# Kernel tuning notes

Measured on AMD Instinct MI355X. Metric: run time of the kernel, lower is better.

Reference implementation:

```python
import jax, jax.numpy as jnp
import numpy as np

DIM = 1024
NUM_HEADS = 16
HEAD_DIM = DIM // NUM_HEADS
SCALE = HEAD_DIM ** -0.5


def setup_inputs() -> dict:
    key = jax.random.key(0)
    ks = jax.random.split(key, 5)
    B, N, C = 2, 2048, DIM
    x = jax.random.normal(ks[0], (B, N, C), dtype=jnp.float32)
    s = 1.0 / np.sqrt(C)
    W_qkv = jax.random.normal(ks[1], (C, 3 * C), dtype=jnp.float32) * s
    b_qkv = jax.random.normal(ks[2], (3 * C,), dtype=jnp.float32) * 0.01
    W_proj = jax.random.normal(ks[3], (C, C), dtype=jnp.float32) * s
    b_proj = jax.random.normal(ks[4], (C,), dtype=jnp.float32) * 0.01
    return {"x": x, "W_qkv": W_qkv, "b_qkv": b_qkv, "W_proj": W_proj, "b_proj": b_proj}


def reference(x, W_qkv, b_qkv, W_proj, b_proj):
    B, N, C = x.shape
    qkv = x @ W_qkv + b_qkv                      # [B, N, 3C]
    qkv = qkv.reshape(B, N, 3, NUM_HEADS, HEAD_DIM)
    qkv = jnp.transpose(qkv, (2, 0, 3, 1, 4))    # [3, B, H, N, hd]
    # Faithful to source quirk: q = k = v = qkv[2]
    v = qkv[2]
    q = v
    k = v
    attn = jnp.einsum('bhnd,bhmd->bhnm', q, k) * SCALE
    attn = jax.nn.softmax(attn, axis=-1)
    out = jnp.einsum('bhnm,bhmd->bhnd', attn, v)  # [B, H, N, hd]
    out = jnp.transpose(out, (0, 2, 1, 3)).reshape(B, N, C)
    return out @ W_proj + b_proj
```

## Files before the change

kernel.cpp:

```cpp
#include <hip/hip_runtime.h>

typedef __bf16    bf16x4 __attribute__((ext_vector_type(4)));
typedef __bf16    bf16x8 __attribute__((ext_vector_type(8)));
typedef _Float16  f16x2  __attribute__((ext_vector_type(2)));
typedef _Float16  f16x4  __attribute__((ext_vector_type(4)));
typedef _Float16  f16x8  __attribute__((ext_vector_type(8)));
typedef float     f32x4  __attribute__((ext_vector_type(4)));

#define MFMA16x16x32 __builtin_amdgcn_mfma_f32_16x16x32_bf16
#define MFMA16x16x16F __builtin_amdgcn_mfma_f32_16x16x16f16

__device__ __forceinline__ void gload_lds16(const void* g, void* l) {
  __builtin_amdgcn_global_load_lds((const __attribute__((address_space(1))) void*)g,
                                   (__attribute__((address_space(3))) void*)l, 16, 0, 0);
}

__device__ __forceinline__ f16x2 pkrtz(float a, float b) {
  return __builtin_bit_cast(f16x2, __builtin_amdgcn_cvt_pkrtz(a, b));
}

__global__ __launch_bounds__(256) void xcast(const float* __restrict__ x,
                                             __bf16* __restrict__ xb) {
  const int gid = blockIdx.x * 256 + threadIdx.x;
  float4 v = ((const float4*)x)[gid];
  bf16x4 o;
  o.x = (__bf16)v.x; o.y = (__bf16)v.y; o.z = (__bf16)v.z; o.w = (__bf16)v.w;
  *(bf16x4*)&xb[(size_t)gid * 4] = o;
}

__global__ __launch_bounds__(256) void prep_transpose(const float* __restrict__ Wqkv,
                                                      const float* __restrict__ Wproj,
                                                      __bf16* __restrict__ WvT,
                                                      __bf16* __restrict__ WpT) {
  __shared__ float tile[64][65];
  const float* src; __bf16* dst; int ld, c0;
  if (blockIdx.z == 0) { src = Wqkv; dst = WvT; ld = 3072; c0 = 2048; }
  else                 { src = Wproj; dst = WpT; ld = 1024; c0 = 0; }
  const int k0 = blockIdx.x * 64, n0 = blockIdx.y * 64;
  const int t = threadIdx.x;
#pragma unroll
  for (int i = 0; i < 4; i++) {
    int idx = t + i * 256; int r = idx >> 4, g = idx & 15;
    float4 v = *(const float4*)&src[(size_t)(k0 + r) * ld + c0 + n0 + g * 4];
    tile[r][g * 4 + 0] = v.x; tile[r][g * 4 + 1] = v.y;
    tile[r][g * 4 + 2] = v.z; tile[r][g * 4 + 3] = v.w;
  }
  __syncthreads();
#pragma unroll
  for (int i = 0; i < 4; i++) {
    int idx = t + i * 256; int n = idx >> 4, g = idx & 15;
    bf16x4 o;
    o.x = (__bf16)tile[g * 4 + 0][n]; o.y = (__bf16)tile[g * 4 + 1][n];
    o.z = (__bf16)tile[g * 4 + 2][n]; o.w = (__bf16)tile[g * 4 + 3][n];
    *(bf16x4*)&dst[(size_t)(n0 + n) * 1024 + k0 + g * 4] = o;
  }
}

__global__ __launch_bounds__(256, 2) void gemm_v(const __bf16* __restrict__ xb,
                                                 const __bf16* __restrict__ WvT,
                                                 const float* __restrict__ bias,
                                                 __bf16* __restrict__ V,
                                                 _Float16* __restrict__ Vt) {
  constexpr int K = 1024;
  __shared__ char lds[2 * 24576];
  const int t = threadIdx.x, w = t >> 6, l = t & 63, lr = l & 15, quad = l >> 4;
  const int wr = w >> 1, wc = w & 1;
  const int m0 = blockIdx.x * 128, n0 = blockIdx.y * 64;

  const int row0 = t >> 3;
  const int scol = (t & 7) ^ (row0 & 7);
  const __bf16* pA = xb  + (size_t)(m0 + row0) * K + scol * 8;
  const __bf16* pB = WvT + (size_t)(n0 + row0) * K + scol * 8;

  f32x4 acc[4][2] = {};
  {
    char* buf = (char*)lds;
    gload_lds16(pA,          buf + t * 16);
    gload_lds16(pA + 32 * K, buf + 4096  + t * 16);
    gload_lds16(pA + 64 * K, buf + 8192  + t * 16);
    gload_lds16(pA + 96 * K, buf + 12288 + t * 16);
    gload_lds16(pB,          buf + 16384 + t * 16);
    gload_lds16(pB + 32 * K, buf + 20480 + t * 16);
  }
  int aoff[4][2], boff[2][2];
#pragma unroll
  for (int mi = 0; mi < 4; mi++)
#pragma unroll
    for (int ks = 0; ks < 2; ks++)
      aoff[mi][ks] = (wr * 64 + mi * 16 + lr) * 128 + (((ks * 4 + quad) ^ (lr & 7)) * 16);
#pragma unroll
  for (int nc = 0; nc < 2; nc++)
#pragma unroll
    for (int ks = 0; ks < 2; ks++)
      boff[nc][ks] = 16384 + (wc * 32 + nc * 16 + lr) * 128 + (((ks * 4 + quad) ^ (lr & 7)) * 16);

  for (int it = 0; it < 16; ++it) {
    __syncthreads();
    if (it + 1 < 16) {
      pA += 64; pB += 64;
      char* buf = (char*)lds + ((it + 1) & 1) * 24576;
      gload_lds16(pA,          buf + t * 16);
      gload_lds16(pA + 32 * K, buf + 4096  + t * 16);
      gload_lds16(pA + 64 * K, buf + 8192  + t * 16);
      gload_lds16(pA + 96 * K, buf + 12288 + t * 16);
      gload_lds16(pB,          buf + 16384 + t * 16);
      gload_lds16(pB + 32 * K, buf + 20480 + t * 16);
    }
    const char* buf = (const char*)lds + (it & 1) * 24576;
    bf16x8 af[4][2], bv[2][2];
#pragma unroll
    for (int mi = 0; mi < 4; mi++)
#pragma unroll
      for (int ks = 0; ks < 2; ks++)
        af[mi][ks] = *(const bf16x8*)(buf + aoff[mi][ks]);
#pragma unroll
    for (int nc = 0; nc < 2; nc++)
#pragma unroll
      for (int ks = 0; ks < 2; ks++)
        bv[nc][ks] = *(const bf16x8*)(buf + boff[nc][ks]);
#pragma unroll
    for (int mi = 0; mi < 4; mi++)
#pragma unroll
      for (int nc = 0; nc < 2; nc++)
#pragma unroll
        for (int ks = 0; ks < 2; ks++)
          acc[mi][nc] = MFMA16x16x32(af[mi][ks], bv[nc][ks], acc[mi][nc], 0, 0, 0);
  }
  const int by = blockIdx.y;
#pragma unroll
  for (int mi = 0; mi < 4; mi++) {
    const int grow0 = m0 + wr * 64 + mi * 16 + quad * 4;
    const int b_ = grow0 >> 11, tok0 = grow0 & 2047;
#pragma unroll
    for (int nc = 0; nc < 2; nc++) {
      const int d = wc * 32 + nc * 16 + lr;
      const int gcol = n0 + d;
      float bb = bias[gcol];
      float v0 = acc[mi][nc][0] + bb, v1 = acc[mi][nc][1] + bb;
      float v2 = acc[mi][nc][2] + bb, v3 = acc[mi][nc][3] + bb;
      V[(size_t)(grow0 + 0) * 1024 + gcol] = (__bf16)v0;
      V[(size_t)(grow0 + 1) * 1024 + gcol] = (__bf16)v1;
      V[(size_t)(grow0 + 2) * 1024 + gcol] = (__bf16)v2;
      V[(size_t)(grow0 + 3) * 1024 + gcol] = (__bf16)v3;
      f16x2 lo = pkrtz(v0, v1), hi = pkrtz(v2, v3);
      f16x4 pv; pv[0] = lo[0]; pv[1] = lo[1]; pv[2] = hi[0]; pv[3] = hi[1];
      *(f16x4*)&Vt[((size_t)(b_ * 16 + by) * 64 + d) * 2048 + tok0] = pv;
    }
  }
}

__global__ __launch_bounds__(256, 2) void gemm_proj(const __bf16* __restrict__ A,
                                                    const __bf16* __restrict__ Bt,
                                                    const float* __restrict__ bias,
                                                    float* __restrict__ outp) {
  constexpr int K = 1024, Nn = 1024;
  __shared__ char lds[2 * 24576];
  const int t = threadIdx.x, w = t >> 6, l = t & 63, lr = l & 15, quad = l >> 4;
  const int wr = w >> 1, wc = w & 1;
  const int m0 = blockIdx.x * 128, n0 = blockIdx.y * 64;

  const int row0 = t >> 3;
  const int scol = (t & 7) ^ (row0 & 7);
  const __bf16* pA = A  + (size_t)(m0 + row0) * K + scol * 8;
  const __bf16* pB = Bt + (size_t)(n0 + row0) * K + scol * 8;

  f32x4 acc[4][2] = {};
  {
    char* buf = (char*)lds;
    gload_lds16(pA,          buf + t * 16);
    gload_lds16(pA + 32 * K, buf + 4096  + t * 16);
    gload_lds16(pA + 64 * K, buf + 8192  + t * 16);
    gload_lds16(pA + 96 * K, buf + 12288 + t * 16);
    gload_lds16(pB,          buf + 16384 + t * 16);
    gload_lds16(pB + 32 * K, buf + 20480 + t * 16);
  }
  int aoff[4][2], boff[2][2];
#pragma unroll
  for (int mi = 0; mi < 4; mi++)
#pragma unroll
    for (int ks = 0; ks < 2; ks++)
      aoff[mi][ks] = (wr * 64 + mi * 16 + lr) * 128 + (((ks * 4 + quad) ^ (lr & 7)) * 16);
#pragma unroll
  for (int nc = 0; nc < 2; nc++)
#pragma unroll
    for (int ks = 0; ks < 2; ks++)
      boff[nc][ks] = 16384 + (wc * 32 + nc * 16 + lr) * 128 + (((ks * 4 + quad) ^ (lr & 7)) * 16);

  for (int it = 0; it < 16; ++it) {
    __syncthreads();
    if (it + 1 < 16) {
      pA += 64; pB += 64;
      char* buf = (char*)lds + ((it + 1) & 1) * 24576;
      gload_lds16(pA,          buf + t * 16);
      gload_lds16(pA + 32 * K, buf + 4096  + t * 16);
      gload_lds16(pA + 64 * K, buf + 8192  + t * 16);
      gload_lds16(pA + 96 * K, buf + 12288 + t * 16);
      gload_lds16(pB,          buf + 16384 + t * 16);
      gload_lds16(pB + 32 * K, buf + 20480 + t * 16);
    }
    const char* buf = (const char*)lds + (it & 1) * 24576;
    bf16x8 af[4][2], bv[2][2];
#pragma unroll
    for (int mi = 0; mi < 4; mi++)
#pragma unroll
      for (int ks = 0; ks < 2; ks++)
        af[mi][ks] = *(const bf16x8*)(buf + aoff[mi][ks]);
#pragma unroll
    for (int nc = 0; nc < 2; nc++)
#pragma unroll
      for (int ks = 0; ks < 2; ks++)
        bv[nc][ks] = *(const bf16x8*)(buf + boff[nc][ks]);
#pragma unroll
    for (int mi = 0; mi < 4; mi++)
#pragma unroll
      for (int nc = 0; nc < 2; nc++)
#pragma unroll
        for (int ks = 0; ks < 2; ks++)
          acc[mi][nc] = MFMA16x16x32(af[mi][ks], bv[nc][ks], acc[mi][nc], 0, 0, 0);
  }
#pragma unroll
  for (int mi = 0; mi < 4; mi++) {
    const int grow0 = m0 + wr * 64 + mi * 16 + quad * 4;
#pragma unroll
    for (int nc = 0; nc < 2; nc++) {
      const int gcol = n0 + wc * 32 + nc * 16 + lr;
      float bb = bias[gcol];
#pragma unroll
      for (int r = 0; r < 4; r++)
        outp[(size_t)(grow0 + r) * Nn + gcol] = acc[mi][nc][r] + bb;
    }
  }
}

__global__ __launch_bounds__(512, 4) void attn_kernel(const __bf16* __restrict__ V,
                                                      const _Float16* __restrict__ Vt,
                                                      __bf16* __restrict__ O) {
  __shared__ char lds[65536];
  const int t = threadIdx.x, w = t >> 6, l = t & 63, lr = l & 15, quad = l >> 4;
  const int bh = blockIdx.x, b = bh >> 4, h = bh & 15;
  const int qb = blockIdx.y * 128 + (w & 3) * 16;
  const int part = w >> 2;

  const __bf16* Vbh = V + (size_t)b * 2048 * 1024 + h * 64;
  const _Float16* Vtbh = Vt + (size_t)bh * 64 * 2048;

  bf16x8 qf[2][2];
#pragma unroll
  for (int sub = 0; sub < 2; sub++)
#pragma unroll
    for (int ks = 0; ks < 2; ks++)
      qf[sub][ks] = *(const bf16x8*)(Vbh + (size_t)(qb + sub * 64 + lr) * 1024 + ks * 32 + quad * 8);

  const int kva = t >> 3, ua = (t & 7) ^ (kva & 7);
  const __bf16* pK0 = Vbh + (size_t)kva * 1024 + ua * 8;
  const __bf16* pK1 = pK0 + (size_t)64 * 1024;
  const int kb_ = t >> 7, d_ = (t >> 1) & 63, qh = (t & 1) ^ ((d_ >> 2) & 1);
  const _Float16* pV0 = Vtbh + (size_t)d_ * 2048 + kb_ * 16 + qh * 8;
  const _Float16* pV1 = pV0 + 64;

  const int koff0 = lr * 128 + ((quad ^ (lr & 7)) * 16);
  const int koff1 = lr * 128 + (((4 + quad) ^ (lr & 7)) * 16);
  const int xq = (quad >> 1) ^ ((lr >> 2) & 1);
  const int voff = lr * 32 + xq * 16 + (quad & 1) * 8;

  f32x4 o[2][4] = {};
  f32x4 l5[2] = {};
  f16x4 ones; ones[0] = ones[1] = ones[2] = ones[3] = (_Float16)1.0f;
  const float Cc = 0.18033688011112042f;
  const float C8 = 11.541560327111707f;

  {
    char* base = lds;
    gload_lds16(pK0, base + t * 16);
    gload_lds16(pV0, base + 8192 + t * 16);
    gload_lds16(pK1, base + 16384 + t * 16);
    gload_lds16(pV1, base + 24576 + t * 16);
  }
  for (int it = 0; it < 16; ++it) {
    __syncthreads();
    if (it + 1 < 16) {
      pK0 += 131072; pK1 += 131072; pV0 += 128; pV1 += 128;
      char* base = lds + ((it + 1) & 1) * 32768;
      gload_lds16(pK0, base + t * 16);
      gload_lds16(pV0, base + 8192 + t * 16);
      gload_lds16(pK1, base + 16384 + t * 16);
      gload_lds16(pV1, base + 24576 + t * 16);
    }
    const char* Kb = lds + (it & 1) * 32768 + part * 16384;
    const char* Vb = Kb + 8192;

    f32x4 s[2][4] = {};
#pragma unroll
    for (int ks = 0; ks < 2; ks++) {
      const int ko = ks ? koff1 : koff0;
#pragma unroll
      for (int rb = 0; rb < 4; rb++) {
        bf16x8 kf = *(const bf16x8*)(Kb + ko + rb * 2048);
        s[0][rb] = MFMA16x16x32(kf, qf[0][ks], s[0][rb], 0, 0, 0);
        s[1][rb] = MFMA16x16x32(kf, qf[1][ks], s[1][rb], 0, 0, 0);
      }
    }

    f16x4 pf[2][4];
#pragma unroll
    for (int sub = 0; sub < 2; sub++)
#pragma unroll
      for (int rb = 0; rb < 4; rb++) {
        float p0 = __builtin_amdgcn_exp2f(s[sub][rb][0] * Cc - C8);
        float p1 = __builtin_amdgcn_exp2f(s[sub][rb][1] * Cc - C8);
        float p2 = __builtin_amdgcn_exp2f(s[sub][rb][2] * Cc - C8);
        float p3 = __builtin_amdgcn_exp2f(s[sub][rb][3] * Cc - C8);
        f16x2 lo = pkrtz(p0, p1);
        f16x2 hi = pkrtz(p2, p3);
        pf[sub][rb][0] = lo[0]; pf[sub][rb][1] = lo[1];
        pf[sub][rb][2] = hi[0]; pf[sub][rb][3] = hi[1];
      }

#pragma unroll
    for (int kb = 0; kb < 4; kb++) {
#pragma unroll
      for (int db = 0; db < 4; db++) {
        f16x4 vf = *(const f16x4*)(Vb + voff + db * 512 + kb * 2048);
        o[0][db] = MFMA16x16x16F(pf[0][kb], vf, o[0][db], 0, 0, 0);
        o[1][db] = MFMA16x16x16F(pf[1][kb], vf, o[1][db], 0, 0, 0);
      }
      l5[0] = MFMA16x16x16F(pf[0][kb], ones, l5[0], 0, 0, 0);
      l5[1] = MFMA16x16x16F(pf[1][kb], ones, l5[1], 0, 0, 0);
    }
  }

  __syncthreads();
  float* xch = (float*)lds;
  if (w >= 4) {
    float* dsto = xch + (w - 4) * 2048;
#pragma unroll
    for (int sub = 0; sub < 2; sub++)
#pragma unroll
      for (int db = 0; db < 4; db++)
        *(f32x4*)&dsto[(sub * 4 + db) * 256 + l * 4] = o[sub][db];
    float* dstl = xch + 8192 + (w - 4) * 512;
    *(f32x4*)&dstl[l * 4] = l5[0];
    *(f32x4*)&dstl[256 + l * 4] = l5[1];
  }
  __syncthreads();
  if (w < 4) {
    const float* srco = xch + w * 2048;
    const float* srcl = xch + 8192 + w * 512;
#pragma unroll
    for (int sub = 0; sub < 2; sub++) {
#pragma unroll
      for (int db = 0; db < 4; db++)
        o[sub][db] += *(const f32x4*)&srco[(sub * 4 + db) * 256 + l * 4];
      l5[sub] += *(const f32x4*)&srcl[sub * 256 + l * 4];
    }
#pragma unroll
    for (int sub = 0; sub < 2; sub++)
#pragma unroll
      for (int r = 0; r < 4; r++) {
        float lv = 1.0f / l5[sub][r];
        int token = b * 2048 + qb + sub * 64 + quad * 4 + r;
#pragma unroll
        for (int db = 0; db < 4; db++)
          O[(size_t)token * 1024 + h * 64 + db * 16 + lr] = (__bf16)(o[sub][db][r] * lv);
      }
  }
}

extern "C" void kernel_launch(void* const* d_in, const int* in_sizes, int n_in,
                              void* d_out, int out_size, void* d_ws, size_t ws_size,
                              hipStream_t stream) {
  (void)in_sizes; (void)n_in; (void)out_size; (void)ws_size;
  const float* x     = (const float*)d_in[0];
  const float* Wqkv  = (const float*)d_in[1];
  const float* bqkv  = (const float*)d_in[2];
  const float* Wproj = (const float*)d_in[3];
  const float* bproj = (const float*)d_in[4];

  char* ws = (char*)d_ws;
  __bf16*    V   = (__bf16*)(ws);
  _Float16*  Vt  = (_Float16*)(ws + (size_t)8  * 1048576);
  __bf16*    Ob  = (__bf16*)(ws + (size_t)16 * 1048576);
  __bf16*    xb  = (__bf16*)(ws + (size_t)16 * 1048576);
  __bf16*    WvT = (__bf16*)(ws + (size_t)24 * 1048576);
  __bf16*    WpT = (__bf16*)(ws + (size_t)26 * 1048576);

  xcast<<<dim3(4096), 256, 0, stream>>>(x, xb);
  prep_transpose<<<dim3(16, 16, 2), 256, 0, stream>>>(Wqkv, Wproj, WvT, WpT);
  gemm_v<<<dim3(32, 16), 256, 0, stream>>>(xb, WvT, bqkv + 2048, V, Vt);
  attn_kernel<<<dim3(32, 16), 512, 0, stream>>>(V, Vt, Ob);
  gemm_proj<<<dim3(32, 16), 256, 0, stream>>>(Ob, WpT, bproj, (float*)d_out);
}
```

Before: 154.0 us.

## Triple-buffer GEMM LDS staging and merge prep kernels into one launch

Both bf16 GEMM kernels move from a double-buffered to a triple-buffered LDS pipeline. Loads are issued two tiles ahead, and each iteration waits on a partial vmcnt followed by a raw s_barrier, replacing a full __syncthreads before each prefetch. The x-cast and weight-transpose kernels are merged into a single prep_all launch, removing one kernel launch. The cost is more LDS per block (72KB), which may limit the two-blocks-per-CU occupancy, and the pipeline depends on correct vmcnt accounting through hand-written waitcnt asm.

New measurement: 155.2 us. About the same (+0.8%).

```diff
diff --git a/kernel.cpp b/kernel.cpp
--- a/kernel.cpp
+++ b/kernel.cpp
@@ -19,25 +19,30 @@
   return __builtin_bit_cast(f16x2, __builtin_amdgcn_cvt_pkrtz(a, b));
 }
 
-__global__ __launch_bounds__(256) void xcast(const float* __restrict__ x,
-                                             __bf16* __restrict__ xb) {
-  const int gid = blockIdx.x * 256 + threadIdx.x;
-  float4 v = ((const float4*)x)[gid];
-  bf16x4 o;
-  o.x = (__bf16)v.x; o.y = (__bf16)v.y; o.z = (__bf16)v.z; o.w = (__bf16)v.w;
-  *(bf16x4*)&xb[(size_t)gid * 4] = o;
-}
-
-__global__ __launch_bounds__(256) void prep_transpose(const float* __restrict__ Wqkv,
-                                                      const float* __restrict__ Wproj,
-                                                      __bf16* __restrict__ WvT,
-                                                      __bf16* __restrict__ WpT) {
+__global__ __launch_bounds__(256) void prep_all(const float* __restrict__ x,
+                                                const float* __restrict__ Wqkv,
+                                                const float* __restrict__ Wproj,
+                                                __bf16* __restrict__ xb,
+                                                __bf16* __restrict__ WvT,
+                                                __bf16* __restrict__ WpT) {
   __shared__ float tile[64][65];
+  const int t = threadIdx.x;
+  if (blockIdx.z == 2) {
+    const int bid = blockIdx.x * 16 + blockIdx.y;
+#pragma unroll
+    for (int c = 0; c < 16; c++) {
+      int gid = (bid * 16 + c) * 256 + t;
+      float4 v = ((const float4*)x)[gid];
+      bf16x4 o;
+      o.x = (__bf16)v.x; o.y = (__bf16)v.y; o.z = (__bf16)v.z; o.w = (__bf16)v.w;
+      *(bf16x4*)&xb[(size_t)gid * 4] = o;
+    }
+    return;
+  }
   const float* src; __bf16* dst; int ld, c0;
   if (blockIdx.z == 0) { src = Wqkv; dst = WvT; ld = 3072; c0 = 2048; }
   else                 { src = Wproj; dst = WpT; ld = 1024; c0 = 0; }
   const int k0 = blockIdx.x * 64, n0 = blockIdx.y * 64;
-  const int t = threadIdx.x;
 #pragma unroll
   for (int i = 0; i < 4; i++) {
     int idx = t + i * 256; int r = idx >> 4, g = idx & 15;
@@ -56,13 +61,24 @@
   }
 }
 
+#define STAGE_TILE(bi, kk)                                            \
+  { char* buf_ = (char*)lds + (bi) * 24576;                           \
+    const __bf16* a_ = pA + (kk) * 64;                                \
+    const __bf16* b_ = pB + (kk) * 64;                                \
+    gload_lds16(a_,          buf_ + t * 16);                          \
+    gload_lds16(a_ + 32 * K, buf_ + 4096  + t * 16);                  \
+    gload_lds16(a_ + 64 * K, buf_ + 8192  + t * 16);                  \
+    gload_lds16(a_ + 96 * K, buf_ + 12288 + t * 16);                  \
+    gload_lds16(b_,          buf_ + 16384 + t * 16);                  \
+    gload_lds16(b_ + 32 * K, buf_ + 20480 + t * 16); }
+
 __global__ __launch_bounds__(256, 2) void gemm_v(const __bf16* __restrict__ xb,
                                                  const __bf16* __restrict__ WvT,
                                                  const float* __restrict__ bias,
                                                  __bf16* __restrict__ V,
                                                  _Float16* __restrict__ Vt) {
   constexpr int K = 1024;
-  __shared__ char lds[2 * 24576];
+  __shared__ char lds[3 * 24576];
   const int t = threadIdx.x, w = t >> 6, l = t & 63, lr = l & 15, quad = l >> 4;
   const int wr = w >> 1, wc = w & 1;
   const int m0 = blockIdx.x * 128, n0 = blockIdx.y * 64;
@@ -73,15 +89,6 @@
   const __bf16* pB = WvT + (size_t)(n0 + row0) * K + scol * 8;
 
   f32x4 acc[4][2] = {};
-  {
-    char* buf = (char*)lds;
-    gload_lds16(pA,          buf + t * 16);
-    gload_lds16(pA + 32 * K, buf + 4096  + t * 16);
-    gload_lds16(pA + 64 * K, buf + 8192  + t * 16);
-    gload_lds16(pA + 96 * K, buf + 12288 + t * 16);
-    gload_lds16(pB,          buf + 16384 + t * 16);
-    gload_lds16(pB + 32 * K, buf + 20480 + t * 16);
-  }
   int aoff[4][2], boff[2][2];
 #pragma unroll
   for (int mi = 0; mi < 4; mi++)
@@ -94,19 +101,15 @@
     for (int ks = 0; ks < 2; ks++)
       boff[nc][ks] = 16384 + (wc * 32 + nc * 16 + lr) * 128 + (((ks * 4 + quad) ^ (lr & 7)) * 16);
 
+  STAGE_TILE(0, 0);
+  STAGE_TILE(1, 1);
   for (int it = 0; it < 16; ++it) {
-    __syncthreads();
-    if (it + 1 < 16) {
-      pA += 64; pB += 64;
-      char* buf = (char*)lds + ((it + 1) & 1) * 24576;
-      gload_lds16(pA,          buf + t * 16);
-      gload_lds16(pA + 32 * K, buf + 4096  + t * 16);
-      gload_lds16(pA + 64 * K, buf + 8192  + t * 16);
-      gload_lds16(pA + 96 * K, buf + 12288 + t * 16);
-      gload_lds16(pB,          buf + 16384 + t * 16);
-      gload_lds16(pB + 32 * K, buf + 20480 + t * 16);
-    }
-    const char* buf = (const char*)lds + (it & 1) * 24576;
+    if (it < 15) { asm volatile("s_waitcnt vmcnt(6)" ::: "memory"); }
+    else         { asm volatile("s_waitcnt vmcnt(0)" ::: "memory"); }
+    __builtin_amdgcn_sched_barrier(0);
+    __builtin_amdgcn_s_barrier();
+    if (it + 2 < 16) STAGE_TILE((it + 2) % 3, it + 2);
+    const char* buf = (const char*)lds + (it % 3) * 24576;
     bf16x8 af[4][2], bv[2][2];
 #pragma unroll
     for (int mi = 0; mi < 4; mi++)
@@ -154,7 +157,7 @@
                                                     const float* __restrict__ bias,
                                                     float* __restrict__ outp) {
   constexpr int K = 1024, Nn = 1024;
-  __shared__ char lds[2 * 24576];
+  __shared__ char lds[3 * 24576];
   const int t = threadIdx.x, w = t >> 6, l = t & 63, lr = l & 15, quad = l >> 4;
   const int wr = w >> 1, wc = w & 1;
   const int m0 = blockIdx.x * 128, n0 = blockIdx.y * 64;
@@ -165,15 +168,6 @@
   const __bf16* pB = Bt + (size_t)(n0 + row0) * K + scol * 8;
 
   f32x4 acc[4][2] = {};
-  {
-    char* buf = (char*)lds;
-    gload_lds16(pA,          buf + t * 16);
-    gload_lds16(pA + 32 * K, buf + 4096  + t * 16);
-    gload_lds16(pA + 64 * K, buf + 8192  + t * 16);
-    gload_lds16(pA + 96 * K, buf + 12288 + t * 16);
-    gload_lds16(pB,          buf + 16384 + t * 16);
-    gload_lds16(pB + 32 * K, buf + 20480 + t * 16);
-  }
   int aoff[4][2], boff[2][2];
 #pragma unroll
   for (int mi = 0; mi < 4; mi++)
@@ -186,19 +180,15 @@
     for (int ks = 0; ks < 2; ks++)
       boff[nc][ks] = 16384 + (wc * 32 + nc * 16 + lr) * 128 + (((ks * 4 + quad) ^ (lr & 7)) * 16);
 
+  STAGE_TILE(0, 0);
+  STAGE_TILE(1, 1);
   for (int it = 0; it < 16; ++it) {
-    __syncthreads();
-    if (it + 1 < 16) {
-      pA += 64; pB += 64;
-      char* buf = (char*)lds + ((it + 1) & 1) * 24576;
-      gload_lds16(pA,          buf + t * 16);
-      gload_lds16(pA + 32 * K, buf + 4096  + t * 16);
-      gload_lds16(pA + 64 * K, buf + 8192  + t * 16);
-      gload_lds16(pA + 96 * K, buf + 12288 + t * 16);
-      gload_lds16(pB,          buf + 16384 + t * 16);
-      gload_lds16(pB + 32 * K, buf + 20480 + t * 16);
-    }
-    const char* buf = (const char*)lds + (it & 1) * 24576;
+    if (it < 15) { asm volatile("s_waitcnt vmcnt(6)" ::: "memory"); }
+    else         { asm volatile("s_waitcnt vmcnt(0)" ::: "memory"); }
+    __builtin_amdgcn_sched_barrier(0);
+    __builtin_amdgcn_s_barrier();
+    if (it + 2 < 16) STAGE_TILE((it + 2) % 3, it + 2);
+    const char* buf = (const char*)lds + (it % 3) * 24576;
     bf16x8 af[4][2], bv[2][2];
 #pragma unroll
     for (int mi = 0; mi < 4; mi++)
@@ -384,8 +374,7 @@
   __bf16*    WvT = (__bf16*)(ws + (size_t)24 * 1048576);
   __bf16*    WpT = (__bf16*)(ws + (size_t)26 * 1048576);
 
-  xcast<<<dim3(4096), 256, 0, stream>>>(x, xb);
-  prep_transpose<<<dim3(16, 16, 2), 256, 0, stream>>>(Wqkv, Wproj, WvT, WpT);
+  prep_all<<<dim3(16, 16, 3), 256, 0, stream>>>(x, Wqkv, Wproj, xb, WvT, WpT);
   gemm_v<<<dim3(32, 16), 256, 0, stream>>>(xb, WvT, bqkv + 2048, V, Vt);
   attn_kernel<<<dim3(32, 16), 512, 0, stream>>>(V, Vt, Ob);
   gemm_proj<<<dim3(32, 16), 256, 0, stream>>>(Ob, WpT, bproj, (float*)d_out);
```
